# Performance work log

Measured on AMD Instinct MI355X. Metric: run time of the kernel, lower is better.

## Reference

```python
import jax, jax.numpy as jnp
import numpy as np

B, D, T, NT, DS, G = 1024, 512, 36, 64, 32, 4
EPS = 1e-5


def setup_inputs() -> dict:
    key = jax.random.key(0)
    ks = jax.random.split(key, 8)
    return {
        "x": jax.random.normal(ks[0], (B, D, T, 1), jnp.float32),
        "y": jax.random.normal(ks[1], (B, D, T, 1), jnp.float32),
        "my_tokens": jax.random.normal(ks[2], (NT, D), jnp.float32) * 0.02,
        "gate": jax.random.normal(ks[3], (1,), jnp.float32) * 0.1,
        "gate_av": jax.random.normal(ks[4], (1,), jnp.float32) * 0.1,
        "w_down": jax.random.normal(ks[5], (DS, D // G), jnp.float32) * 0.05,  # Conv2d(512->32,1,groups=4) weight [32,128,1,1] squeezed
        "w_up": jax.random.normal(ks[6], (D, DS // G), jnp.float32) * 0.05,    # Conv2d(32->512,1,groups=4) weight [512,8,1,1] squeezed
        "bn1_g": jnp.ones((DS,), jnp.float32), "bn1_b": jnp.zeros((DS,), jnp.float32),
        "bn2_g": jnp.ones((D,), jnp.float32), "bn2_b": jnp.zeros((D,), jnp.float32),
        "lnb_g": jnp.ones((D,), jnp.float32), "lnb_b": jnp.zeros((D,), jnp.float32),
        "lnp_g": jnp.ones((D,), jnp.float32), "lnp_b": jnp.zeros((D,), jnp.float32),
    }


def _layernorm(h, g, b):  # normalize last dim
    mu = jnp.mean(h, axis=-1, keepdims=True)
    var = jnp.var(h, axis=-1, keepdims=True)
    return (h - mu) * jax.lax.rsqrt(var + EPS) * g + b


def _batchnorm(z, g, b):  # z: [B,C,T], training-mode batch stats over (B,T)
    mu = jnp.mean(z, axis=(0, 2), keepdims=True)
    var = jnp.var(z, axis=(0, 2), keepdims=True)
    return (z - mu) * jax.lax.rsqrt(var + EPS) * g[None, :, None] + b[None, :, None]


def reference(x, y, my_tokens, gate, gate_av, w_down, w_up,
              bn1_g, bn1_b, bn2_g, bn2_b, lnb_g, lnb_b, lnp_g, lnp_b):
    xs = x[..., 0]  # [B,D,T]
    ys = y[..., 0]  # [B,D,T]
    # token <- y cross attention
    att_y2tk = jax.nn.softmax(jnp.einsum('td,bds->bts', my_tokens, ys), axis=-1)  # [B,NT,T]
    rep = my_tokens[None] + jnp.einsum('bts,bds->btd', att_y2tk, ys)  # [B,NT,D]
    # x <- token cross attention
    att_tk2x = jax.nn.softmax(jnp.einsum('bds,btd->bst', xs, rep), axis=-1)  # [B,T,NT]
    x_res = jnp.einsum('bst,btd->bsd', att_tk2x, rep)  # [B,T,D]
    xc = xs + gate_av[0] * jnp.swapaxes(x_res, 1, 2)  # [B,D,T]
    # ln_before over channel dim
    h = jnp.swapaxes(_layernorm(jnp.swapaxes(xc, 1, 2), lnb_g, lnb_b), 1, 2)  # [B,D,T]
    # grouped 1x1 down conv
    hg = h.reshape(h.shape[0], G, D // G, T)
    z = jnp.einsum('bgct,goc->bgot', hg, w_down.reshape(G, DS // G, D // G)).reshape(h.shape[0], DS, T)
    z = jax.nn.relu(_batchnorm(z, bn1_g, bn1_b))
    # grouped 1x1 up conv
    zg = z.reshape(z.shape[0], G, DS // G, T)
    o = jnp.einsum('bgct,goc->bgot', zg, w_up.reshape(G, D // G, DS // G)).reshape(z.shape[0], D, T)
    o = _batchnorm(o, bn2_g, bn2_b)
    o = jnp.swapaxes(_layernorm(jnp.swapaxes(o, 1, 2), lnp_g, lnp_b), 1, 2)
    return (gate[0] * o)[..., None]  # [B,D,T,1]
```

## Files before the change

### kernel.cpp

```cpp
#include <hip/hip_runtime.h>

#define B_ 1024
#define D_ 512
#define T_ 36
#define NT_ 64
#define DS_ 32
#define EPS_ 1e-5f

typedef float f32x4 __attribute__((ext_vector_type(4)));
typedef __bf16 bf16x8 __attribute__((ext_vector_type(8)));
typedef unsigned short u16x8 __attribute__((ext_vector_type(8)));

#define DEVI static __device__ __forceinline__
#define MFMA16 __builtin_amdgcn_mfma_f32_16x16x32_bf16

DEVI unsigned short f2bf(float f) { return __builtin_bit_cast(unsigned short, (__bf16)f); }
DEVI float bf2f(unsigned short h) { return (float)__builtin_bit_cast(__bf16, h); }

DEVI unsigned swz(int row, int col) {
    return (unsigned)(row * 1024 + ((2 * col) ^ ((row & 7) << 4)));
}

#define OFF_YST 0
#define OFF_XST 49152
#define OFF_SC  98304
#define OFF_A1  109056
#define OFF_A1T 118272
#define OFF_A2  125184
#define OFF_GT  132096
#define OFF_W   139008
#define K1_LDS  145920

__global__ __launch_bounds__(512)
void k0_prepack(const float* __restrict__ tok, const float* __restrict__ wd,
                unsigned short* __restrict__ tokbf, unsigned short* __restrict__ tokT,
                unsigned short* __restrict__ wdd)
{
    int i = blockIdx.x * 512 + threadIdx.x;
    if (i < 32768) {
        tokbf[i] = f2bf(tok[i]);
    } else if (i < 65536) {
        int j = i - 32768; int d = j >> 6, t = j & 63;
        tokT[j] = f2bf(tok[t * 512 + d]);
    } else if (i < 81920) {
        int j = i - 65536; int o = j >> 9, dd = j & 511;
        wdd[j] = ((dd >> 7) == (o >> 3)) ? f2bf(wd[o * 128 + (dd & 127)]) : (unsigned short)0;
    }
}

__global__ __launch_bounds__(1024, 4)
void k1_fused(const float* __restrict__ x, const float* __restrict__ y,
              const unsigned short* __restrict__ tokbf, const unsigned short* __restrict__ tokT,
              const float* __restrict__ gav_p, const unsigned short* __restrict__ wdd,
              const float* __restrict__ lnbg, const float* __restrict__ lnbb,
              float* __restrict__ z_pre)
{
    extern __shared__ char lds[];
    float* sc = (float*)(lds + OFF_SC);
    unsigned short* a1  = (unsigned short*)(lds + OFF_A1);
    unsigned short* a1t = (unsigned short*)(lds + OFF_A1T);
    unsigned short* a2  = (unsigned short*)(lds + OFF_A2);
    unsigned short* gt  = (unsigned short*)(lds + OFF_GT);
    unsigned short* wb  = (unsigned short*)(lds + OFF_W);

    const int b    = blockIdx.x;
    const int tid  = threadIdx.x;
    const int lane = tid & 63;
    const int w    = tid >> 6;
    const int l15  = lane & 15;
    const int l4   = lane >> 4;

    const float* yb = y + b * (D_ * T_);
    const float* xb = x + b * (D_ * T_);

    {
        unsigned* z1 = (unsigned*)(lds + OFF_YST + 36 * 1024);
        unsigned* z2 = (unsigned*)(lds + OFF_XST + 36 * 1024);
        for (int i = tid; i < 3072; i += 1024) { z1[i] = 0u; z2[i] = 0u; }
        unsigned* z3 = (unsigned*)(lds + OFF_A1);
        for (int i = tid; i < 9216; i += 1024) z3[i] = 0u;
    }
    for (int ww = tid; ww < 1152; ww += 1024) {
        int isx = (ww >= 576) ? 1 : 0;
        int u = isx ? (ww - 576) : ww;
        const float* src = isx ? xb : yb;
        char* dst = lds + (isx ? OFF_XST : OFF_YST);
        int dblk = u / 9, s4 = u - dblk * 9;
        int s0 = s4 * 4;
        const float* bp = src + dblk * 8 * T_ + s0;
        u16x8 u0, u1, u2, u3;
        #pragma unroll
        for (int r = 0; r < 8; ++r) {
            f32x4 v = *(const f32x4*)(bp + r * T_);
            u0[r] = f2bf(v[0]); u1[r] = f2bf(v[1]);
            u2[r] = f2bf(v[2]); u3[r] = f2bf(v[3]);
        }
        *(u16x8*)(dst + swz(s0 + 0, dblk * 8)) = u0;
        *(u16x8*)(dst + swz(s0 + 1, dblk * 8)) = u1;
        *(u16x8*)(dst + swz(s0 + 2, dblk * 8)) = u2;
        *(u16x8*)(dst + swz(s0 + 3, dblk * 8)) = u3;
    }
    __syncthreads();

    for (int tile = w; tile < 21; tile += 16) {
        f32x4 acc = {0.f, 0.f, 0.f, 0.f};
        if (tile < 12) {
            int mt = tile / 3, nt = tile % 3;
            int trow = mt * 16 + l15, srow = nt * 16 + l15;
            for (int ks = 0; ks < 16; ++ks) {
                int k0 = ks * 32 + l4 * 8;
                bf16x8 af = *(const bf16x8*)(tokbf + trow * 512 + k0);
                bf16x8 bv = *(const bf16x8*)(lds + OFF_YST + swz(srow, k0));
                acc = MFMA16(af, bv, acc, 0, 0, 0);
            }
            if (srow < T_) {
                #pragma unroll
                for (int j = 0; j < 4; ++j)
                    sc[(mt * 16 + l4 * 4 + j) * 42 + srow] = acc[j];
            }
        } else {
            int g = tile - 12;
            int mt = g / 3, nt = g % 3;
            int arow = mt * 16 + l15, brow = nt * 16 + l15;
            for (int ks = 0; ks < 16; ++ks) {
                int k0 = ks * 32 + l4 * 8;
                bf16x8 af = *(const bf16x8*)(lds + OFF_XST + swz(arow, k0));
                bf16x8 bv = *(const bf16x8*)(lds + OFF_YST + swz(brow, k0));
                acc = MFMA16(af, bv, acc, 0, 0, 0);
            }
            #pragma unroll
            for (int j = 0; j < 4; ++j)
                gt[(mt * 16 + l4 * 4 + j) * 72 + brow] = f2bf(acc[j]);
        }
    }
    __syncthreads();

    {
        int t = tid >> 4, l16 = tid & 15;
        const float* scp = sc + t * 42;
        float v0 = scp[l16];
        float v1 = scp[l16 + 16];
        float v2 = (l16 < 4) ? scp[l16 + 32] : -1e30f;
        float m = fmaxf(fmaxf(v0, v1), v2);
        #pragma unroll
        for (int off = 1; off < 16; off <<= 1) m = fmaxf(m, __shfl_xor(m, off));
        float e0 = __expf(v0 - m), e1 = __expf(v1 - m);
        float e2 = (l16 < 4) ? __expf(v2 - m) : 0.f;
        float ssum = e0 + e1 + e2;
        #pragma unroll
        for (int off = 1; off < 16; off <<= 1) ssum += __shfl_xor(ssum, off);
        float inv = 1.f / ssum;
        unsigned short h0 = f2bf(e0 * inv), h1 = f2bf(e1 * inv);
        a1[t * 72 + l16] = h0;       a1[t * 72 + l16 + 16] = h1;
        a1t[l16 * 72 + t] = h0;      a1t[(l16 + 16) * 72 + t] = h1;
        if (l16 < 4) {
            unsigned short h2 = f2bf(e2 * inv);
            a1[t * 72 + l16 + 32] = h2;
            a1t[(l16 + 32) * 72 + t] = h2;
        }
    }
    __syncthreads();

    if (w < 12) {
        int mt = w / 3, nt = w % 3;
        int trow = mt * 16 + l15, srow = nt * 16 + l15;
        f32x4 acc = {0.f, 0.f, 0.f, 0.f};
        for (int ks = 0; ks < 16; ++ks) {
            int k0 = ks * 32 + l4 * 8;
            bf16x8 af = *(const bf16x8*)(tokbf + trow * 512 + k0);
            bf16x8 bv = *(const bf16x8*)(lds + OFF_XST + swz(srow, k0));
            acc = MFMA16(af, bv, acc, 0, 0, 0);
        }
        #pragma unroll
        for (int ks = 0; ks < 2; ++ks) {
            int k0 = ks * 32 + l4 * 8;
            bf16x8 af = *(const bf16x8*)(a1 + trow * 72 + k0);
            bf16x8 bv = *(const bf16x8*)(gt + srow * 72 + k0);
            acc = MFMA16(af, bv, acc, 0, 0, 0);
        }
        if (srow < T_) {
            #pragma unroll
            for (int j = 0; j < 4; ++j)
                sc[(mt * 16 + l4 * 4 + j) * 42 + srow] = acc[j];
        }
    }
    __syncthreads();

    if (tid < 768) {
        int s = tid >> 4, l16 = tid & 15;
        if (s < T_) {
            float v0 = sc[(l16) * 42 + s];
            float v1 = sc[(l16 + 16) * 42 + s];
            float v2 = sc[(l16 + 32) * 42 + s];
            float v3 = sc[(l16 + 48) * 42 + s];
            float m = fmaxf(fmaxf(v0, v1), fmaxf(v2, v3));
            #pragma unroll
            for (int off = 1; off < 16; off <<= 1) m = fmaxf(m, __shfl_xor(m, off));
            float e0 = __expf(v0 - m), e1 = __expf(v1 - m), e2 = __expf(v2 - m), e3 = __expf(v3 - m);
            float ssum = e0 + e1 + e2 + e3;
            #pragma unroll
            for (int off = 1; off < 16; off <<= 1) ssum += __shfl_xor(ssum, off);
            float inv = 1.f / ssum;
            a2[s * 72 + l16]      = f2bf(e0 * inv);
            a2[s * 72 + l16 + 16] = f2bf(e1 * inv);
            a2[s * 72 + l16 + 32] = f2bf(e2 * inv);
            a2[s * 72 + l16 + 48] = f2bf(e3 * inv);
        }
    }
    __syncthreads();

    if (w < 9) {
        int mt = w / 3, nt = w % 3;
        f32x4 acc = {0.f, 0.f, 0.f, 0.f};
        #pragma unroll
        for (int ks = 0; ks < 2; ++ks) {
            int k0 = ks * 32 + l4 * 8;
            bf16x8 af = *(const bf16x8*)(a2 + (mt * 16 + l15) * 72 + k0);
            bf16x8 bv = *(const bf16x8*)(a1t + (nt * 16 + l15) * 72 + k0);
            acc = MFMA16(af, bv, acc, 0, 0, 0);
        }
        #pragma unroll
        for (int j = 0; j < 4; ++j)
            wb[(mt * 16 + l4 * 4 + j) * 72 + nt * 16 + l15] = f2bf(acc[j]);
    }
    __syncthreads();

    {
        const float gav = gav_p[0];
        f32x4 acc[2][3];
        #pragma unroll
        for (int mi = 0; mi < 2; ++mi)
            #pragma unroll
            for (int n = 0; n < 3; ++n) acc[mi][n] = (f32x4){0.f, 0.f, 0.f, 0.f};

        bf16x8 aT[2][2], aY[2][2];
        #pragma unroll
        for (int mi = 0; mi < 2; ++mi) {
            int d = (2 * w + mi) * 16 + l15;
            aT[mi][0] = *(const bf16x8*)(tokT + d * 64 + l4 * 8);
            aT[mi][1] = *(const bf16x8*)(tokT + d * 64 + 32 + l4 * 8);
            const float* yrow = yb + d * T_;
            f32x4 p0 = *(const f32x4*)(yrow + l4 * 8);
            f32x4 p1 = *(const f32x4*)(yrow + l4 * 8 + 4);
            bf16x8 t0, t1;
            #pragma unroll
            for (int j = 0; j < 4; ++j) { t0[j] = (__bf16)p0[j]; t0[4 + j] = (__bf16)p1[j]; }
            if (l4 == 0) {
                f32x4 p2 = *(const f32x4*)(yrow + 32);
                #pragma unroll
                for (int j = 0; j < 4; ++j) { t1[j] = (__bf16)p2[j]; t1[4 + j] = (__bf16)0.f; }
            } else {
                #pragma unroll
                for (int j = 0; j < 8; ++j) t1[j] = (__bf16)0.f;
            }
            aY[mi][0] = t0; aY[mi][1] = t1;
        }
        #pragma unroll
        for (int n = 0; n < 3; ++n) {
            int srow = n * 16 + l15;
            bf16x8 b20 = *(const bf16x8*)(a2 + srow * 72 + l4 * 8);
            bf16x8 b21 = *(const bf16x8*)(a2 + srow * 72 + 32 + l4 * 8);
            bf16x8 bw0 = *(const bf16x8*)(wb + srow * 72 + l4 * 8);
            bf16x8 bw1 = *(const bf16x8*)(wb + srow * 72 + 32 + l4 * 8);
            #pragma unroll
            for (int mi = 0; mi < 2; ++mi) {
                acc[mi][n] = MFMA16(aT[mi][0], b20, acc[mi][n], 0, 0, 0);
                acc[mi][n] = MFMA16(aT[mi][1], b21, acc[mi][n], 0, 0, 0);
                acc[mi][n] = MFMA16(aY[mi][0], bw0, acc[mi][n], 0, 0, 0);
                acc[mi][n] = MFMA16(aY[mi][1], bw1, acc[mi][n], 0, 0, 0);
            }
        }

        float* red = sc;
        float rs_[3] = {0.f, 0.f, 0.f}, rq_[3] = {0.f, 0.f, 0.f};
        #pragma unroll
        for (int mi = 0; mi < 2; ++mi) {
            #pragma unroll
            for (int n = 0; n < 3; ++n) {
                int s = n * 16 + l15;
                if (s < T_) {
                    #pragma unroll
                    for (int j = 0; j < 4; ++j) {
                        int d = (2 * w + mi) * 16 + l4 * 4 + j;
                        float xsv = bf2f(*(const unsigned short*)(lds + OFF_XST + swz(s, d)));
                        float v = xsv + gav * acc[mi][n][j];
                        acc[mi][n][j] = v;
                        rs_[n] += v; rq_[n] += v * v;
                    }
                }
            }
        }
        #pragma unroll
        for (int n = 0; n < 3; ++n) {
            rs_[n] += __shfl_xor(rs_[n], 16); rq_[n] += __shfl_xor(rq_[n], 16);
            rs_[n] += __shfl_xor(rs_[n], 32); rq_[n] += __shfl_xor(rq_[n], 32);
        }
        if (l4 == 0) {
            #pragma unroll
            for (int n = 0; n < 3; ++n) {
                int s = n * 16 + l15;
                if (s < T_) { red[s * 16 + w] = rs_[n]; red[768 + s * 16 + w] = rq_[n]; }
            }
        }
        __syncthreads();
        if (tid < T_) {
            int s = tid; float S = 0.f, Q = 0.f;
            #pragma unroll
            for (int q = 0; q < 16; ++q) { S += red[s * 16 + q]; Q += red[768 + s * 16 + q]; }
            float mu = S * (1.f / 512.f);
            float var = Q * (1.f / 512.f) - mu * mu;
            red[1536 + s] = mu; red[1584 + s] = rsqrtf(var + EPS_);
        }
        __syncthreads();

        float lg[2][4], lbv[2][4];
        #pragma unroll
        for (int mi = 0; mi < 2; ++mi)
            #pragma unroll
            for (int j = 0; j < 4; ++j) {
                int d = (2 * w + mi) * 16 + l4 * 4 + j;
                lg[mi][j] = lnbg[d]; lbv[mi][j] = lnbb[d];
            }
        #pragma unroll
        for (int mi = 0; mi < 2; ++mi) {
            #pragma unroll
            for (int n = 0; n < 3; ++n) {
                int s = n * 16 + l15;
                if (s < T_) {
                    float mu = red[1536 + s], rsg = red[1584 + s];
                    #pragma unroll
                    for (int j = 0; j < 4; ++j) {
                        int d = (2 * w + mi) * 16 + l4 * 4 + j;
                        *(unsigned short*)(lds + OFF_YST + swz(s, d)) =
                            f2bf((acc[mi][n][j] - mu) * rsg * lg[mi][j] + lbv[mi][j]);
                    }
                }
            }
        }
    }
    __syncthreads();

    if (w < 6) {
        int mt = w / 3, nt = w % 3;
        int orow = mt * 16 + l15, srow = nt * 16 + l15;
        f32x4 acc = {0.f, 0.f, 0.f, 0.f};
        for (int ks = 0; ks < 16; ++ks) {
            int k0 = ks * 32 + l4 * 8;
            bf16x8 af = *(const bf16x8*)(wdd + orow * 512 + k0);
            bf16x8 bv = *(const bf16x8*)(lds + OFF_YST + swz(srow, k0));
            acc = MFMA16(af, bv, acc, 0, 0, 0);
        }
        if (srow < T_) {
            #pragma unroll
            for (int j = 0; j < 4; ++j)
                z_pre[b * (DS_ * T_) + (mt * 16 + l4 * 4 + j) * T_ + srow] = acc[j];
        }
    }
}

__global__ __launch_bounds__(256)
void k3a_bn1part(const float* __restrict__ z_pre, float* __restrict__ p3)
{
    __shared__ float rbuf[4][2];
    int blk = blockIdx.x;
    int o = blk & 31, sl = blk >> 5;
    int tid = threadIdx.x;
    float S = 0.f, Q = 0.f;
    for (int i = tid; i < 64 * T_; i += 256) {
        int bb = sl * 64 + i / T_, t = i - (i / T_) * T_;
        float v = z_pre[bb * (DS_ * T_) + o * T_ + t];
        S += v; Q += v * v;
    }
    #pragma unroll
    for (int off = 1; off < 64; off <<= 1) { S += __shfl_xor(S, off); Q += __shfl_xor(Q, off); }
    int ww = tid >> 6;
    if ((tid & 63) == 0) { rbuf[ww][0] = S; rbuf[ww][1] = Q; }
    __syncthreads();
    if (tid == 0) {
        float s2 = 0.f, q2 = 0.f;
        for (int i = 0; i < 4; ++i) { s2 += rbuf[i][0]; q2 += rbuf[i][1]; }
        p3[blk * 2] = s2; p3[blk * 2 + 1] = q2;
    }
}

__global__ __launch_bounds__(64)
void k3b_bn1stats(const float* __restrict__ p3, float* __restrict__ st1)
{
    int o = threadIdx.x;
    if (o < 32) {
        float S = 0.f, Q = 0.f;
        for (int sl = 0; sl < 16; ++sl) {
            S += p3[((sl << 5) | o) * 2];
            Q += p3[((sl << 5) | o) * 2 + 1];
        }
        float mu = S / 36864.f;
        float var = Q / 36864.f - mu * mu;
        st1[o] = mu; st1[32 + o] = rsqrtf(var + EPS_);
    }
}

__global__ __launch_bounds__(256)
void k4m_moments(const float* __restrict__ z_pre, const float* __restrict__ st1,
                 const float* __restrict__ g1p, const float* __restrict__ b1p,
                 float* __restrict__ m4)
{
    __shared__ float zr[32][40];
    int blk = blockIdx.x, tid = threadIdx.x;
    int c2 = tid & 7, c1 = (tid >> 3) & 7, g = tid >> 6;
    int ch1 = g * 8 + c1, ch2 = g * 8 + c2;
    float acc = 0.f, asum = 0.f;
    for (int bi = 0; bi < 16; ++bi) {
        int b = blk * 16 + bi;
        __syncthreads();
        for (int i = tid; i < DS_ * T_; i += 256) {
            int o = i / T_, t = i - o * T_;
            float v = z_pre[b * (DS_ * T_) + i];
            zr[o][t] = fmaxf(0.f, (v - st1[o]) * st1[32 + o] * g1p[o] + b1p[o]);
        }
        __syncthreads();
        for (int t = 0; t < T_; ++t) {
            float a = zr[ch1][t], b2 = zr[ch2][t];
            acc += a * b2;
            asum += a;
        }
    }
    m4[blk * 288 + tid] = acc;
    if (c1 == c2) m4[blk * 288 + 256 + g * 8 + c1] = asum;
}

__global__ __launch_bounds__(512)
void k4s_bn2stats(const float* __restrict__ m4, const float* __restrict__ wu,
                  float* __restrict__ st2)
{
    __shared__ float M2[256], mz[32];
    int tid = threadIdx.x;
    if (tid < 256) {
        float S = 0.f;
        for (int k = 0; k < 64; ++k) S += m4[k * 288 + tid];
        M2[tid] = S * (1.f / 36864.f);
    } else if (tid < 288) {
        int j = tid - 256;
        float S = 0.f;
        for (int k = 0; k < 64; ++k) S += m4[k * 288 + 256 + j];
        mz[j] = S * (1.f / 36864.f);
    }
    __syncthreads();
    int d = tid, g = d >> 7;
    float wr[8];
    #pragma unroll
    for (int c = 0; c < 8; ++c) wr[c] = wu[d * 8 + c];
    float mu2 = 0.f;
    #pragma unroll
    for (int c = 0; c < 8; ++c) mu2 += wr[c] * mz[g * 8 + c];
    float e2 = 0.f;
    #pragma unroll
    for (int c = 0; c < 8; ++c)
        #pragma unroll
        for (int c2 = 0; c2 < 8; ++c2)
            e2 += wr[c] * wr[c2] * M2[g * 64 + c * 8 + c2];
    st2[d] = mu2;
    st2[512 + d] = rsqrtf(e2 - mu2 * mu2 + EPS_);
}

#define K5_LDS 47888
__global__ __launch_bounds__(512, 6)
void k5_final(const float* __restrict__ z_pre, const float* __restrict__ st1,
              const float* __restrict__ g1p, const float* __restrict__ b1p,
              const float* __restrict__ wu, const float* __restrict__ st2,
              const float* __restrict__ g2p, const float* __restrict__ b2p,
              const float* __restrict__ lnpg, const float* __restrict__ lnpb,
              const float* __restrict__ gate_p, float* __restrict__ out)
{
    extern __shared__ char lds[];
    unsigned short* o_f = (unsigned short*)lds;
    float* zrT = (float*)(lds + 41984);
    int b = blockIdx.x;
    int tid = threadIdx.x;

    for (int i = tid; i < DS_ * T_; i += 512) {
        int o = i / T_, s = i - o * T_;
        float v = z_pre[b * (DS_ * T_) + i];
        zrT[s * 41 + o] = fmaxf(0.f, (v - st1[o]) * st1[32 + o] * g1p[o] + b1p[o]);
    }
    __syncthreads();

    for (int i = tid; i < D_ * T_; i += 512) {
        int d = i / T_, t = i - d * T_;
        const float* zp = &zrT[t * 41 + (d >> 7) * 8];
        const float* wp = &wu[d * 8];
        f32x4 w0 = *(const f32x4*)wp;
        f32x4 w1 = *(const f32x4*)(wp + 4);
        float acc = zp[0]*w0[0] + zp[1]*w0[1] + zp[2]*w0[2] + zp[3]*w0[3]
                  + zp[4]*w1[0] + zp[5]*w1[1] + zp[6]*w1[2] + zp[7]*w1[3];
        o_f[d * 41 + t] = f2bf((acc - st2[d]) * st2[512 + d] * g2p[d] + b2p[d]);
    }
    __syncthreads();

    int w = tid >> 6, lane = tid & 63;
    float gate = gate_p[0];
    for (int t = w; t < T_; t += 8) {
        float S = 0.f, Q = 0.f;
        float v[8];
        #pragma unroll
        for (int i2 = 0; i2 < 8; ++i2) {
            float vv = bf2f(o_f[(i2 * 64 + lane) * 41 + t]);
            v[i2] = vv; S += vv; Q += vv * vv;
        }
        #pragma unroll
        for (int off = 1; off < 64; off <<= 1) { S += __shfl_xor(S, off); Q += __shfl_xor(Q, off); }
        float mu = S * (1.f / 512.f);
        float var = Q * (1.f / 512.f) - mu * mu;
        float rs = rsqrtf(var + EPS_);
        #pragma unroll
        for (int i2 = 0; i2 < 8; ++i2) {
            int d = i2 * 64 + lane;
            o_f[d * 41 + t] = f2bf(gate * ((v[i2] - mu) * rs * lnpg[d] + lnpb[d]));
        }
    }
    __syncthreads();

    float* ob = out + b * (D_ * T_);
    for (int i = tid; i < D_ * T_; i += 512) {
        int d = i / T_, t = i - d * T_;
        ob[i] = bf2f(o_f[d * 41 + t]);
    }
}

extern "C" void kernel_launch(void* const* d_in, const int* in_sizes, int n_in,
                              void* d_out, int out_size, void* d_ws, size_t ws_size,
                              hipStream_t stream)
{
    (void)in_sizes; (void)n_in; (void)out_size; (void)ws_size;
    const float* x    = (const float*)d_in[0];
    const float* y    = (const float*)d_in[1];
    const float* tok  = (const float*)d_in[2];
    const float* gate = (const float*)d_in[3];
    const float* gav  = (const float*)d_in[4];
    const float* wd   = (const float*)d_in[5];
    const float* wu   = (const float*)d_in[6];
    const float* bn1g = (const float*)d_in[7];
    const float* bn1b = (const float*)d_in[8];
    const float* bn2g = (const float*)d_in[9];
    const float* bn2b = (const float*)d_in[10];
    const float* lnbg = (const float*)d_in[11];
    const float* lnbb = (const float*)d_in[12];
    const float* lnpg = (const float*)d_in[13];
    const float* lnpb = (const float*)d_in[14];
    float* out = (float*)d_out;

    char* ws = (char*)d_ws;
    float* z_pre          = (float*)ws;
    float* st1            = (float*)(ws + 4718592);
    unsigned short* tokbf = (unsigned short*)(ws + 4719104);
    unsigned short* tokT  = (unsigned short*)(ws + 4784640);
    unsigned short* wdd   = (unsigned short*)(ws + 4850176);
    float* p3             = (float*)(ws + 4882944);
    float* m4             = (float*)(ws + 4887040);
    float* st2            = (float*)(ws + 4960768);

    hipFuncSetAttribute((const void*)k1_fused, hipFuncAttributeMaxDynamicSharedMemorySize, K1_LDS);
    hipFuncSetAttribute((const void*)k5_final, hipFuncAttributeMaxDynamicSharedMemorySize, K5_LDS);

    k0_prepack<<<160, 512, 0, stream>>>(tok, wd, tokbf, tokT, wdd);
    k1_fused<<<B_, 1024, K1_LDS, stream>>>(x, y, tokbf, tokT, gav, wdd, lnbg, lnbb, z_pre);
    k3a_bn1part<<<512, 256, 0, stream>>>(z_pre, p3);
    k3b_bn1stats<<<1, 64, 0, stream>>>(p3, st1);
    k4m_moments<<<64, 256, 0, stream>>>(z_pre, st1, bn1g, bn1b, m4);
    k4s_bn2stats<<<1, 512, 0, stream>>>(m4, wu, st2);
    k5_final<<<B_, 512, K5_LDS, stream>>>(z_pre, st1, bn1g, bn1b, wu, st2, bn2g, bn2b,
                                          lnpg, lnpb, gate, out);
}
```

Before: 201.3 us.

## Materialize rep explicitly in LDS instead of folding through attention product

```diff
diff --git a/kernel.cpp b/kernel.cpp
--- a/kernel.cpp
+++ b/kernel.cpp
@@ -21,19 +21,16 @@
     return (unsigned)(row * 1024 + ((2 * col) ^ ((row & 7) << 4)));
 }
 
-#define OFF_YST 0
-#define OFF_XST 49152
-#define OFF_SC  98304
-#define OFF_A1  109056
-#define OFF_A1T 118272
-#define OFF_A2  125184
-#define OFF_GT  132096
-#define OFF_W   139008
-#define K1_LDS  145920
+#define OFF_XST 73728
+#define OFF_SC  122880
+#define OFF_A1  133632
+#define OFF_A2  142848
+#define OFF_GT  149760
+#define K1_LDS  156672
 
 __global__ __launch_bounds__(512)
 void k0_prepack(const float* __restrict__ tok, const float* __restrict__ wd,
-                unsigned short* __restrict__ tokbf, unsigned short* __restrict__ tokT,
+                unsigned short* __restrict__ tokbf, float* __restrict__ tokTf,
                 unsigned short* __restrict__ wdd)
 {
     int i = blockIdx.x * 512 + threadIdx.x;
@@ -41,7 +38,7 @@
         tokbf[i] = f2bf(tok[i]);
     } else if (i < 65536) {
         int j = i - 32768; int d = j >> 6, t = j & 63;
-        tokT[j] = f2bf(tok[t * 512 + d]);
+        tokTf[j] = tok[t * 512 + d];
     } else if (i < 81920) {
         int j = i - 65536; int o = j >> 9, dd = j & 511;
         wdd[j] = ((dd >> 7) == (o >> 3)) ? f2bf(wd[o * 128 + (dd & 127)]) : (unsigned short)0;
@@ -50,18 +47,16 @@
 
 __global__ __launch_bounds__(1024, 4)
 void k1_fused(const float* __restrict__ x, const float* __restrict__ y,
-              const unsigned short* __restrict__ tokbf, const unsigned short* __restrict__ tokT,
+              const unsigned short* __restrict__ tokbf, const float* __restrict__ tokTf,
               const float* __restrict__ gav_p, const unsigned short* __restrict__ wdd,
               const float* __restrict__ lnbg, const float* __restrict__ lnbb,
               float* __restrict__ z_pre)
 {
     extern __shared__ char lds[];
     float* sc = (float*)(lds + OFF_SC);
-    unsigned short* a1  = (unsigned short*)(lds + OFF_A1);
-    unsigned short* a1t = (unsigned short*)(lds + OFF_A1T);
-    unsigned short* a2  = (unsigned short*)(lds + OFF_A2);
-    unsigned short* gt  = (unsigned short*)(lds + OFF_GT);
-    unsigned short* wb  = (unsigned short*)(lds + OFF_W);
+    unsigned short* a1 = (unsigned short*)(lds + OFF_A1);
+    unsigned short* a2 = (unsigned short*)(lds + OFF_A2);
+    unsigned short* gt = (unsigned short*)(lds + OFF_GT);
 
     const int b    = blockIdx.x;
     const int tid  = threadIdx.x;
@@ -74,17 +69,17 @@
     const float* xb = x + b * (D_ * T_);
 
     {
-        unsigned* z1 = (unsigned*)(lds + OFF_YST + 36 * 1024);
+        unsigned* z1 = (unsigned*)(lds + 36 * 1024);
         unsigned* z2 = (unsigned*)(lds + OFF_XST + 36 * 1024);
         for (int i = tid; i < 3072; i += 1024) { z1[i] = 0u; z2[i] = 0u; }
         unsigned* z3 = (unsigned*)(lds + OFF_A1);
-        for (int i = tid; i < 9216; i += 1024) z3[i] = 0u;
+        for (int i = tid; i < 5760; i += 1024) z3[i] = 0u;
     }
     for (int ww = tid; ww < 1152; ww += 1024) {
         int isx = (ww >= 576) ? 1 : 0;
         int u = isx ? (ww - 576) : ww;
         const float* src = isx ? xb : yb;
-        char* dst = lds + (isx ? OFF_XST : OFF_YST);
+        char* dst = lds + (isx ? OFF_XST : 0);
         int dblk = u / 9, s4 = u - dblk * 9;
         int s0 = s4 * 4;
         const float* bp = src + dblk * 8 * T_ + s0;
@@ -103,34 +98,44 @@
     __syncthreads();
 
     for (int tile = w; tile < 21; tile += 16) {
-        f32x4 acc = {0.f, 0.f, 0.f, 0.f};
+        f32x4 acc0 = {0.f,0.f,0.f,0.f}, acc1 = {0.f,0.f,0.f,0.f};
         if (tile < 12) {
             int mt = tile / 3, nt = tile % 3;
             int trow = mt * 16 + l15, srow = nt * 16 + l15;
-            for (int ks = 0; ks < 16; ++ks) {
-                int k0 = ks * 32 + l4 * 8;
-                bf16x8 af = *(const bf16x8*)(tokbf + trow * 512 + k0);
-                bf16x8 bv = *(const bf16x8*)(lds + OFF_YST + swz(srow, k0));
-                acc = MFMA16(af, bv, acc, 0, 0, 0);
-            }
+            #pragma unroll
+            for (int ks = 0; ks < 16; ks += 2) {
+                int ka = ks * 32 + l4 * 8, kb = ka + 32;
+                acc0 = MFMA16(*(const bf16x8*)(tokbf + trow * 512 + ka),
+                              *(const bf16x8*)(lds + swz(srow, ka)), acc0, 0, 0, 0);
+                acc1 = MFMA16(*(const bf16x8*)(tokbf + trow * 512 + kb),
+                              *(const bf16x8*)(lds + swz(srow, kb)), acc1, 0, 0, 0);
+            }
+            f32x4 acc = acc0 + acc1;
             if (srow < T_) {
                 #pragma unroll
                 for (int j = 0; j < 4; ++j)
                     sc[(mt * 16 + l4 * 4 + j) * 42 + srow] = acc[j];
             }
         } else {
-            int g = tile - 12;
-            int mt = g / 3, nt = g % 3;
+            int g2 = tile - 12;
+            int mt = g2 / 3, nt = g2 % 3;
             int arow = mt * 16 + l15, brow = nt * 16 + l15;
-            for (int ks = 0; ks < 16; ++ks) {
-                int k0 = ks * 32 + l4 * 8;
-                bf16x8 af = *(const bf16x8*)(lds + OFF_XST + swz(arow, k0));
-                bf16x8 bv = *(const bf16x8*)(lds + OFF_YST + swz(brow, k0));
-                acc = MFMA16(af, bv, acc, 0, 0, 0);
-            }
-            #pragma unroll
-            for (int j = 0; j < 4; ++j)
-                gt[(mt * 16 + l4 * 4 + j) * 72 + brow] = f2bf(acc[j]);
+            #pragma unroll
+            for (int ks = 0; ks < 16; ks += 2) {
+                int ka = ks * 32 + l4 * 8, kb = ka + 32;
+                acc0 = MFMA16(*(const bf16x8*)(lds + OFF_XST + swz(arow, ka)),
+                              *(const bf16x8*)(lds + swz(brow, ka)), acc0, 0, 0, 0);
+                acc1 = MFMA16(*(const bf16x8*)(lds + OFF_XST + swz(arow, kb)),
+                              *(const bf16x8*)(lds + swz(brow, kb)), acc1, 0, 0, 0);
+            }
+            f32x4 acc = acc0 + acc1;
+            if (brow < T_) {
+                #pragma unroll
+                for (int j = 0; j < 4; ++j) {
+                    int gr = mt * 16 + l4 * 4 + j;
+                    if (gr < T_) gt[gr * 72 + brow] = f2bf(acc[j]);
+                }
+            }
         }
     }
     __syncthreads();
@@ -150,34 +155,60 @@
         #pragma unroll
         for (int off = 1; off < 16; off <<= 1) ssum += __shfl_xor(ssum, off);
         float inv = 1.f / ssum;
-        unsigned short h0 = f2bf(e0 * inv), h1 = f2bf(e1 * inv);
-        a1[t * 72 + l16] = h0;       a1[t * 72 + l16 + 16] = h1;
-        a1t[l16 * 72 + t] = h0;      a1t[(l16 + 16) * 72 + t] = h1;
-        if (l16 < 4) {
-            unsigned short h2 = f2bf(e2 * inv);
-            a1[t * 72 + l16 + 32] = h2;
-            a1t[(l16 + 32) * 72 + t] = h2;
-        }
-    }
-    __syncthreads();
-
+        a1[t * 72 + l16]      = f2bf(e0 * inv);
+        a1[t * 72 + l16 + 16] = f2bf(e1 * inv);
+        if (l16 < 4) a1[t * 72 + l16 + 32] = f2bf(e2 * inv);
+    }
+    __syncthreads();
+
+    #pragma unroll
+    for (int i = 0; i < 8; ++i) {
+        int q = w + 16 * i;
+        int dt = q & 31, tt = q >> 5;
+        int dbase = dt * 16, tbase = tt * 16;
+        const float* yrow = yb + (dbase + l15) * T_;
+        f32x4 p0 = *(const f32x4*)(yrow + l4 * 8);
+        f32x4 p1 = *(const f32x4*)(yrow + l4 * 8 + 4);
+        bf16x8 fa0, fa1;
+        #pragma unroll
+        for (int j = 0; j < 4; ++j) { fa0[j] = (__bf16)p0[j]; fa0[4 + j] = (__bf16)p1[j]; }
+        if (l4 == 0) {
+            f32x4 p2 = *(const f32x4*)(yrow + 32);
+            #pragma unroll
+            for (int j = 0; j < 4; ++j) { fa1[j] = (__bf16)p2[j]; fa1[4 + j] = (__bf16)0.f; }
+        } else {
+            #pragma unroll
+            for (int j = 0; j < 8; ++j) fa1[j] = (__bf16)0.f;
+        }
+        bf16x8 fb0 = *(const bf16x8*)(a1 + (tbase + l15) * 72 + l4 * 8);
+        bf16x8 fb1 = *(const bf16x8*)(a1 + (tbase + l15) * 72 + 32 + l4 * 8);
+        f32x4 acc = {0.f,0.f,0.f,0.f};
+        acc = MFMA16(fa0, fb0, acc, 0, 0, 0);
+        acc = MFMA16(fa1, fb1, acc, 0, 0, 0);
+        #pragma unroll
+        for (int j = 0; j < 4; ++j) {
+            int d = dbase + l4 * 4 + j;
+            float val = tokTf[d * 64 + tbase + l15] + acc[j];
+            *(unsigned short*)(lds + d * 144 + 2 * (tbase + l15)) = f2bf(val);
+        }
+    }
     if (w < 12) {
         int mt = w / 3, nt = w % 3;
         int trow = mt * 16 + l15, srow = nt * 16 + l15;
-        f32x4 acc = {0.f, 0.f, 0.f, 0.f};
-        for (int ks = 0; ks < 16; ++ks) {
-            int k0 = ks * 32 + l4 * 8;
-            bf16x8 af = *(const bf16x8*)(tokbf + trow * 512 + k0);
-            bf16x8 bv = *(const bf16x8*)(lds + OFF_XST + swz(srow, k0));
-            acc = MFMA16(af, bv, acc, 0, 0, 0);
-        }
-        #pragma unroll
-        for (int ks = 0; ks < 2; ++ks) {
-            int k0 = ks * 32 + l4 * 8;
-            bf16x8 af = *(const bf16x8*)(a1 + trow * 72 + k0);
-            bf16x8 bv = *(const bf16x8*)(gt + srow * 72 + k0);
-            acc = MFMA16(af, bv, acc, 0, 0, 0);
-        }
+        f32x4 acc0 = {0.f,0.f,0.f,0.f}, acc1 = {0.f,0.f,0.f,0.f};
+        #pragma unroll
+        for (int ks = 0; ks < 16; ks += 2) {
+            int ka = ks * 32 + l4 * 8, kb = ka + 32;
+            acc0 = MFMA16(*(const bf16x8*)(tokbf + trow * 512 + ka),
+                          *(const bf16x8*)(lds + OFF_XST + swz(srow, ka)), acc0, 0, 0, 0);
+            acc1 = MFMA16(*(const bf16x8*)(tokbf + trow * 512 + kb),
+                          *(const bf16x8*)(lds + OFF_XST + swz(srow, kb)), acc1, 0, 0, 0);
+        }
+        acc0 = MFMA16(*(const bf16x8*)(a1 + trow * 72 + l4 * 8),
+                      *(const bf16x8*)(gt + srow * 72 + l4 * 8), acc0, 0, 0, 0);
+        acc1 = MFMA16(*(const bf16x8*)(a1 + trow * 72 + 32 + l4 * 8),
+                      *(const bf16x8*)(gt + srow * 72 + 32 + l4 * 8), acc1, 0, 0, 0);
+        f32x4 acc = acc0 + acc1;
         if (srow < T_) {
             #pragma unroll
             for (int j = 0; j < 4; ++j)
@@ -186,154 +217,94 @@
     }
     __syncthreads();
 
-    if (tid < 768) {
+    if (tid < 576) {
         int s = tid >> 4, l16 = tid & 15;
-        if (s < T_) {
-            float v0 = sc[(l16) * 42 + s];
-            float v1 = sc[(l16 + 16) * 42 + s];
-            float v2 = sc[(l16 + 32) * 42 + s];
-            float v3 = sc[(l16 + 48) * 42 + s];
-            float m = fmaxf(fmaxf(v0, v1), fmaxf(v2, v3));
-            #pragma unroll
-            for (int off = 1; off < 16; off <<= 1) m = fmaxf(m, __shfl_xor(m, off));
-            float e0 = __expf(v0 - m), e1 = __expf(v1 - m), e2 = __expf(v2 - m), e3 = __expf(v3 - m);
-            float ssum = e0 + e1 + e2 + e3;
-            #pragma unroll
-            for (int off = 1; off < 16; off <<= 1) ssum += __shfl_xor(ssum, off);
-            float inv = 1.f / ssum;
-            a2[s * 72 + l16]      = f2bf(e0 * inv);
-            a2[s * 72 + l16 + 16] = f2bf(e1 * inv);
-            a2[s * 72 + l16 + 32] = f2bf(e2 * inv);
-            a2[s * 72 + l16 + 48] = f2bf(e3 * inv);
-        }
-    }
-    __syncthreads();
-
-    if (w < 9) {
-        int mt = w / 3, nt = w % 3;
-        f32x4 acc = {0.f, 0.f, 0.f, 0.f};
-        #pragma unroll
-        for (int ks = 0; ks < 2; ++ks) {
-            int k0 = ks * 32 + l4 * 8;
-            bf16x8 af = *(const bf16x8*)(a2 + (mt * 16 + l15) * 72 + k0);
-            bf16x8 bv = *(const bf16x8*)(a1t + (nt * 16 + l15) * 72 + k0);
-            acc = MFMA16(af, bv, acc, 0, 0, 0);
-        }
-        #pragma unroll
-        for (int j = 0; j < 4; ++j)
-            wb[(mt * 16 + l4 * 4 + j) * 72 + nt * 16 + l15] = f2bf(acc[j]);
+        float v0 = sc[(l16     ) * 42 + s];
+        float v1 = sc[(l16 + 16) * 42 + s];
+        float v2 = sc[(l16 + 32) * 42 + s];
+        float v3 = sc[(l16 + 48) * 42 + s];
+        float m = fmaxf(fmaxf(v0, v1), fmaxf(v2, v3));
+        #pragma unroll
+        for (int off = 1; off < 16; off <<= 1) m = fmaxf(m, __shfl_xor(m, off));
+        float e0 = __expf(v0 - m), e1 = __expf(v1 - m), e2 = __expf(v2 - m), e3 = __expf(v3 - m);
+        float ssum = e0 + e1 + e2 + e3;
+        #pragma unroll
+        for (int off = 1; off < 16; off <<= 1) ssum += __shfl_xor(ssum, off);
+        float inv = 1.f / ssum;
+        a2[s * 72 + l16]      = f2bf(e0 * inv);
+        a2[s * 72 + l16 + 16] = f2bf(e1 * inv);
+        a2[s * 72 + l16 + 32] = f2bf(e2 * inv);
+        a2[s * 72 + l16 + 48] = f2bf(e3 * inv);
     }
     __syncthreads();
 
     {
         const float gav = gav_p[0];
-        f32x4 acc[2][3];
-        #pragma unroll
-        for (int mi = 0; mi < 2; ++mi)
-            #pragma unroll
-            for (int n = 0; n < 3; ++n) acc[mi][n] = (f32x4){0.f, 0.f, 0.f, 0.f};
-
-        bf16x8 aT[2][2], aY[2][2];
-        #pragma unroll
-        for (int mi = 0; mi < 2; ++mi) {
-            int d = (2 * w + mi) * 16 + l15;
-            aT[mi][0] = *(const bf16x8*)(tokT + d * 64 + l4 * 8);
-            aT[mi][1] = *(const bf16x8*)(tokT + d * 64 + 32 + l4 * 8);
-            const float* yrow = yb + d * T_;
-            f32x4 p0 = *(const f32x4*)(yrow + l4 * 8);
-            f32x4 p1 = *(const f32x4*)(yrow + l4 * 8 + 4);
-            bf16x8 t0, t1;
-            #pragma unroll
-            for (int j = 0; j < 4; ++j) { t0[j] = (__bf16)p0[j]; t0[4 + j] = (__bf16)p1[j]; }
-            if (l4 == 0) {
-                f32x4 p2 = *(const f32x4*)(yrow + 32);
+        float* red = sc;
+        f32x4 acc6[6];
+        #pragma unroll
+        for (int i = 0; i < 6; ++i) {
+            int q = w * 6 + i;
+            int dt = q & 31, st = q >> 5;
+            int dbase = dt * 16, sbase = st * 16;
+            f32x4 acc = {0.f,0.f,0.f,0.f};
+            #pragma unroll
+            for (int ks = 0; ks < 2; ++ks) {
+                int k0 = ks * 32 + l4 * 8;
+                bf16x8 af = *(const bf16x8*)(lds + (dbase + l15) * 144 + k0 * 2);
+                bf16x8 bv = *(const bf16x8*)(a2 + (sbase + l15) * 72 + k0);
+                acc = MFMA16(af, bv, acc, 0, 0, 0);
+            }
+            acc6[i] = acc;
+        }
+        #pragma unroll
+        for (int i = 0; i < 6; ++i) {
+            int q = w * 6 + i;
+            int dt = q & 31, st = q >> 5;
+            int dbase = dt * 16, sbase = st * 16;
+            int s = sbase + l15;
+            float rsum = 0.f, rsq = 0.f;
+            if (s < T_) {
                 #pragma unroll
-                for (int j = 0; j < 4; ++j) { t1[j] = (__bf16)p2[j]; t1[4 + j] = (__bf16)0.f; }
-            } else {
-                #pragma unroll
-                for (int j = 0; j < 8; ++j) t1[j] = (__bf16)0.f;
-            }
-            aY[mi][0] = t0; aY[mi][1] = t1;
-        }
-        #pragma unroll
-        for (int n = 0; n < 3; ++n) {
-            int srow = n * 16 + l15;
-            bf16x8 b20 = *(const bf16x8*)(a2 + srow * 72 + l4 * 8);
-            bf16x8 b21 = *(const bf16x8*)(a2 + srow * 72 + 32 + l4 * 8);
-            bf16x8 bw0 = *(const bf16x8*)(wb + srow * 72 + l4 * 8);
-            bf16x8 bw1 = *(const bf16x8*)(wb + srow * 72 + 32 + l4 * 8);
-            #pragma unroll
-            for (int mi = 0; mi < 2; ++mi) {
-                acc[mi][n] = MFMA16(aT[mi][0], b20, acc[mi][n], 0, 0, 0);
-                acc[mi][n] = MFMA16(aT[mi][1], b21, acc[mi][n], 0, 0, 0);
-                acc[mi][n] = MFMA16(aY[mi][0], bw0, acc[mi][n], 0, 0, 0);
-                acc[mi][n] = MFMA16(aY[mi][1], bw1, acc[mi][n], 0, 0, 0);
-            }
-        }
-
-        float* red = sc;
-        float rs_[3] = {0.f, 0.f, 0.f}, rq_[3] = {0.f, 0.f, 0.f};
-        #pragma unroll
-        for (int mi = 0; mi < 2; ++mi) {
-            #pragma unroll
-            for (int n = 0; n < 3; ++n) {
-                int s = n * 16 + l15;
-                if (s < T_) {
-                    #pragma unroll
-                    for (int j = 0; j < 4; ++j) {
-                        int d = (2 * w + mi) * 16 + l4 * 4 + j;
-                        float xsv = bf2f(*(const unsigned short*)(lds + OFF_XST + swz(s, d)));
-                        float v = xsv + gav * acc[mi][n][j];
-                        acc[mi][n][j] = v;
-                        rs_[n] += v; rq_[n] += v * v;
-                    }
+                for (int j = 0; j < 4; ++j) {
+                    int d = dbase + l4 * 4 + j;
+                    float xsv = bf2f(*(const unsigned short*)(lds + OFF_XST + swz(s, d)));
+                    float v = xsv + gav * acc6[i][j];
+                    acc6[i][j] = v;
+                    rsum += v; rsq += v * v;
                 }
             }
-        }
-        #pragma unroll
-        for (int n = 0; n < 3; ++n) {
-            rs_[n] += __shfl_xor(rs_[n], 16); rq_[n] += __shfl_xor(rq_[n], 16);
-            rs_[n] += __shfl_xor(rs_[n], 32); rq_[n] += __shfl_xor(rq_[n], 32);
-        }
-        if (l4 == 0) {
-            #pragma unroll
-            for (int n = 0; n < 3; ++n) {
-                int s = n * 16 + l15;
-                if (s < T_) { red[s * 16 + w] = rs_[n]; red[768 + s * 16 + w] = rq_[n]; }
+            rsum += __shfl_xor(rsum, 16); rsq += __shfl_xor(rsq, 16);
+            rsum += __shfl_xor(rsum, 32); rsq += __shfl_xor(rsq, 32);
+            if (s < T_ && l4 == 0) {
+                red[s * 32 + dt] = rsum;
+                red[1152 + s * 32 + dt] = rsq;
             }
         }
         __syncthreads();
         if (tid < T_) {
             int s = tid; float S = 0.f, Q = 0.f;
             #pragma unroll
-            for (int q = 0; q < 16; ++q) { S += red[s * 16 + q]; Q += red[768 + s * 16 + q]; }
+            for (int q = 0; q < 32; ++q) { S += red[s * 32 + q]; Q += red[1152 + s * 32 + q]; }
             float mu = S * (1.f / 512.f);
             float var = Q * (1.f / 512.f) - mu * mu;
-            red[1536 + s] = mu; red[1584 + s] = rsqrtf(var + EPS_);
+            red[2304 + s] = mu; red[2340 + s] = rsqrtf(var + EPS_);
         }
         __syncthreads();
-
-        float lg[2][4], lbv[2][4];
-        #pragma unroll
-        for (int mi = 0; mi < 2; ++mi)
-            #pragma unroll
-            for (int j = 0; j < 4; ++j) {
-                int d = (2 * w + mi) * 16 + l4 * 4 + j;
-                lg[mi][j] = lnbg[d]; lbv[mi][j] = lnbb[d];
-            }
-        #pragma unroll
-        for (int mi = 0; mi < 2; ++mi) {
-            #pragma unroll
-            for (int n = 0; n < 3; ++n) {
-                int s = n * 16 + l15;
-                if (s < T_) {
-                    float mu = red[1536 + s], rsg = red[1584 + s];
-                    #pragma unroll
-                    for (int j = 0; j < 4; ++j) {
-                        int d = (2 * w + mi) * 16 + l4 * 4 + j;
-                        *(unsigned short*)(lds + OFF_YST + swz(s, d)) =
-                            f2bf((acc[mi][n][j] - mu) * rsg * lg[mi][j] + lbv[mi][j]);
-                    }
+        #pragma unroll
+        for (int i = 0; i < 6; ++i) {
+            int q = w * 6 + i;
+            int dt = q & 31, st = q >> 5;
+            int dbase = dt * 16, sbase = st * 16;
+            int s = sbase + l15;
+            if (s < T_) {
+                float mu = red[2304 + s], rsig = red[2340 + s];
+                #pragma unroll
+                for (int j = 0; j < 4; ++j) {
+                    int d = dbase + l4 * 4 + j;
+                    float g = lnbg[d], bb2 = lnbb[d];
+                    *(unsigned short*)(lds + OFF_XST + swz(s, d)) =
+                        f2bf((acc6[i][j] - mu) * rsig * g + bb2);
                 }
             }
         }
@@ -343,13 +314,16 @@
     if (w < 6) {
         int mt = w / 3, nt = w % 3;
         int orow = mt * 16 + l15, srow = nt * 16 + l15;
-        f32x4 acc = {0.f, 0.f, 0.f, 0.f};
-        for (int ks = 0; ks < 16; ++ks) {
-            int k0 = ks * 32 + l4 * 8;
-            bf16x8 af = *(const bf16x8*)(wdd + orow * 512 + k0);
-            bf16x8 bv = *(const bf16x8*)(lds + OFF_YST + swz(srow, k0));
-            acc = MFMA16(af, bv, acc, 0, 0, 0);
-        }
+        f32x4 acc0 = {0.f,0.f,0.f,0.f}, acc1 = {0.f,0.f,0.f,0.f};
+        #pragma unroll
+        for (int ks = 0; ks < 16; ks += 2) {
+            int ka = ks * 32 + l4 * 8, kb = ka + 32;
+            acc0 = MFMA16(*(const bf16x8*)(wdd + orow * 512 + ka),
+                          *(const bf16x8*)(lds + OFF_XST + swz(srow, ka)), acc0, 0, 0, 0);
+            acc1 = MFMA16(*(const bf16x8*)(wdd + orow * 512 + kb),
+                          *(const bf16x8*)(lds + OFF_XST + swz(srow, kb)), acc1, 0, 0, 0);
+        }
+        f32x4 acc = acc0 + acc1;
         if (srow < T_) {
             #pragma unroll
             for (int j = 0; j < 4; ++j)
@@ -409,8 +383,8 @@
     int c2 = tid & 7, c1 = (tid >> 3) & 7, g = tid >> 6;
     int ch1 = g * 8 + c1, ch2 = g * 8 + c2;
     float acc = 0.f, asum = 0.f;
-    for (int bi = 0; bi < 16; ++bi) {
-        int b = blk * 16 + bi;
+    for (int bi = 0; bi < 8; ++bi) {
+        int b = blk * 8 + bi;
         __syncthreads();
         for (int i = tid; i < DS_ * T_; i += 256) {
             int o = i / T_, t = i - o * T_;
@@ -436,12 +410,12 @@
     int tid = threadIdx.x;
     if (tid < 256) {
         float S = 0.f;
-        for (int k = 0; k < 64; ++k) S += m4[k * 288 + tid];
+        for (int k = 0; k < 128; ++k) S += m4[k * 288 + tid];
         M2[tid] = S * (1.f / 36864.f);
     } else if (tid < 288) {
         int j = tid - 256;
         float S = 0.f;
-        for (int k = 0; k < 64; ++k) S += m4[k * 288 + 256 + j];
+        for (int k = 0; k < 128; ++k) S += m4[k * 288 + 256 + j];
         mz[j] = S * (1.f / 36864.f);
     }
     __syncthreads();
@@ -552,20 +526,20 @@
     float* z_pre          = (float*)ws;
     float* st1            = (float*)(ws + 4718592);
     unsigned short* tokbf = (unsigned short*)(ws + 4719104);
-    unsigned short* tokT  = (unsigned short*)(ws + 4784640);
-    unsigned short* wdd   = (unsigned short*)(ws + 4850176);
-    float* p3             = (float*)(ws + 4882944);
-    float* m4             = (float*)(ws + 4887040);
-    float* st2            = (float*)(ws + 4960768);
+    float* tokTf          = (float*)(ws + 4784640);
+    unsigned short* wdd   = (unsigned short*)(ws + 4915712);
+    float* p3             = (float*)(ws + 4948480);
+    float* m4             = (float*)(ws + 4952576);
+    float* st2            = (float*)(ws + 5100032);
 
     hipFuncSetAttribute((const void*)k1_fused, hipFuncAttributeMaxDynamicSharedMemorySize, K1_LDS);
     hipFuncSetAttribute((const void*)k5_final, hipFuncAttributeMaxDynamicSharedMemorySize, K5_LDS);
 
-    k0_prepack<<<160, 512, 0, stream>>>(tok, wd, tokbf, tokT, wdd);
-    k1_fused<<<B_, 1024, K1_LDS, stream>>>(x, y, tokbf, tokT, gav, wdd, lnbg, lnbb, z_pre);
+    k0_prepack<<<160, 512, 0, stream>>>(tok, wd, tokbf, tokTf, wdd);
+    k1_fused<<<B_, 1024, K1_LDS, stream>>>(x, y, tokbf, tokTf, gav, wdd, lnbg, lnbb, z_pre);
     k3a_bn1part<<<512, 256, 0, stream>>>(z_pre, p3);
     k3b_bn1stats<<<1, 64, 0, stream>>>(p3, st1);
-    k4m_moments<<<64, 256, 0, stream>>>(z_pre, st1, bn1g, bn1b, m4);
+    k4m_moments<<<128, 256, 0, stream>>>(z_pre, st1, bn1g, bn1b, m4);
     k4s_bn2stats<<<1, 512, 0, stream>>>(m4, wu, st2);
     k5_final<<<B_, 512, K5_LDS, stream>>>(z_pre, st1, bn1g, bn1b, wu, st2, bn2g, bn2b,
                                           lnpg, lnpb, gate, out);
```

After: 212.9 us. +5.8%, slower.
